# Kernel optimization log

Measured on AMD Instinct MI355X. Metric: run time of the kernel, lower is better.

Reference implementation:

```python
import jax, jax.numpy as jnp
import numpy as np
from jax import lax

H = 1024        # lstm_hidden_size
V = 512         # action_vocab_size
WV = 300        # word_vec_size
S = 64          # step_num
N = 512         # entity_num


def setup_inputs() -> dict:
    key = jax.random.key(0)
    ks = jax.random.split(key, 16)
    s = 0.02
    return {
        "video_vectors": jax.random.normal(ks[0], (1, S, H), jnp.float32),
        "entity_vectors": jax.random.normal(ks[1], (N, H), jnp.float32),
        # action_selector: Linear(H,H) -> ReLU -> Dropout(eval: identity) -> Linear(H,V) -> Sigmoid
        "A1w": jax.random.normal(ks[2], (H, H), jnp.float32) * s,
        "A1b": jnp.zeros((H,), jnp.float32),
        "A2w": jax.random.normal(ks[3], (V, H), jnp.float32) * s,
        "A2b": jnp.zeros((V,), jnp.float32),
        "action_emb": jax.random.normal(ks[4], (V, WV), jnp.float32) * s,
        "W1w": jax.random.normal(ks[5], (H, H), jnp.float32) * s,
        "W1b": jnp.zeros((H,), jnp.float32),
        "W2w": jax.random.normal(ks[6], (H, H + V), jnp.float32) * s,
        "W2b": jnp.zeros((H,), jnp.float32),
        "W3w": jax.random.normal(ks[7], (3, H), jnp.float32) * s,
        "W3b": jnp.zeros((3,), jnp.float32),
        "W4w": jax.random.normal(ks[8], (1, WV), jnp.float32) * s,
        "W4b": jnp.zeros((1,), jnp.float32),
    }


def _forward(video_vectors, entity_vectors, A1w, A1b, A2w, A2b, action_emb,
             W1w, W1b, W2w, W2b, W3w, W3b, W4w, W4b):
    vv = video_vectors[0]                       # [S, H]
    n = entity_vectors.shape[0]

    def step(carry, v_ac):
        ev, prev_ent_attn = carry               # ev: [N, H], prev: [N]
        # action selector (dropout is identity in eval)
        h = jax.nn.relu(v_ac @ A1w.T + A1b)
        ac_prob = jax.nn.sigmoid(h @ A2w.T + A2b)        # [V]
        bar_ft = (ac_prob / ac_prob.sum()) @ action_emb  # [WV]
        hat_ht = jax.nn.relu(v_ac @ W1w.T + W1b)         # [H]
        w2v = jnp.concatenate([hat_ht, ac_prob]) @ W2w.T + W2b  # [H]
        ent_prob = jax.nn.sigmoid(ev @ w2v)              # [N]
        choice = jax.nn.softmax(hat_ht @ W3w.T + W3b)    # [3]
        attn = choice[0] * ent_prob + choice[1] * prev_ent_attn  # (choice[2]*0)
        bar_et = (attn / attn.sum()) @ ev                # [H]
        scal = bar_ft @ W4w[0] + W4b[0]                  # scalar (W4(bar_ft))
        kt = jax.nn.relu(scal * bar_et)                  # [H]
        ev_new = attn[:, None] * kt[None, :] + (1.0 - attn)[:, None] * ev  # [N, H]
        return (ev_new, ent_prob), (ent_prob, ac_prob, bar_et, ev_new, bar_ft)

    init = (entity_vectors, jnp.zeros((n,), entity_vectors.dtype))
    _, (ent_probs, ac_probs, step_ent, step_all, step_act) = lax.scan(step, init, vv)
    return ent_probs, ac_probs, step_ent, step_all, step_act


def reference(video_vectors, entity_vectors, A1w, A1b, A2w, A2b, action_emb,
              W1w, W1b, W2w, W2b, W3w, W3b, W4w, W4b):
    return _forward(video_vectors, entity_vectors, A1w, A1b, A2w, A2b, action_emb,
                    W1w, W1b, W2w, W2b, W3w, W3b, W4w, W4b)
```

## Files before the change

### kernel.cpp

```cpp
#include <hip/hip_runtime.h>

#define H  1024
#define V  512
#define WV 300
#define S  64
#define N  512

#define WS_HALL   0
#define WS_CAT    (S*H)
#define WS_W2V    (WS_CAT + S*1536)
#define WS_CHOICE (WS_W2V + S*H)
#define WS_SCAL   (WS_CHOICE + 2*S)
#define WS_ACSUM  (WS_SCAL + S)
#define WS_KT     (WS_ACSUM + S)
#define WS_ATT    (WS_KT + S*H)
#define WS_ACCUM  (WS_ATT + S*N)
#define WS_ASUM   (WS_ACCUM + 3*H)
#define WS_CTR    (WS_ASUM + 4)

#define OUT_EP   0
#define OUT_AC   (S*N)
#define OUT_SE   (S*N + S*V)
#define OUT_ALL  (OUT_SE + S*H)
#define OUT_ACT  (OUT_ALL + (size_t)S*N*H)

__device__ __forceinline__ float wave_reduce(float v) {
#pragma unroll
  for (int m = 32; m > 0; m >>= 1) v += __shfl_xor(v, m, 64);
  return v;
}
__device__ __forceinline__ float dot4(float4 a, float4 b) {
  return a.x*b.x + a.y*b.y + a.z*b.z + a.w*b.w;
}

#define KC 64
__global__ __launch_bounds__(256) void gemmNT(
    const float* __restrict__ X, int ldx,
    const float* __restrict__ W, const float* __restrict__ bias,
    int K, int act,
    float* __restrict__ out1, int ld1,
    float* __restrict__ out2, int ld2) {
  __shared__ float Xs[64][KC + 4];
  __shared__ float Ws[64][KC + 4];
  const int tid = threadIdx.x;
  const int tm = tid >> 5, tn = tid & 31;
  const int jbase = blockIdx.x * 64;
  float acc[8][2];
#pragma unroll
  for (int i = 0; i < 8; ++i) acc[i][0] = acc[i][1] = 0.f;
  const int lr = tid >> 2;
  const int lc = (tid & 3) * 16;
  for (int k0 = 0; k0 < K; k0 += KC) {
    const float4* xp = (const float4*)(X + (size_t)lr * ldx + k0 + lc);
    const float4* wp = (const float4*)(W + (size_t)(jbase + lr) * K + k0 + lc);
    float4 xv0 = xp[0], xv1 = xp[1], xv2 = xp[2], xv3 = xp[3];
    float4 wv0 = wp[0], wv1 = wp[1], wv2 = wp[2], wv3 = wp[3];
    __syncthreads();
    *(float4*)&Xs[lr][lc +  0] = xv0; *(float4*)&Xs[lr][lc +  4] = xv1;
    *(float4*)&Xs[lr][lc +  8] = xv2; *(float4*)&Xs[lr][lc + 12] = xv3;
    *(float4*)&Ws[lr][lc +  0] = wv0; *(float4*)&Ws[lr][lc +  4] = wv1;
    *(float4*)&Ws[lr][lc +  8] = wv2; *(float4*)&Ws[lr][lc + 12] = wv3;
    __syncthreads();
#pragma unroll
    for (int kk = 0; kk < KC; kk += 4) {
      float4 w0 = *(const float4*)&Ws[tn][kk];
      float4 w1 = *(const float4*)&Ws[tn + 32][kk];
#pragma unroll
      for (int i = 0; i < 8; ++i) {
        float4 x = *(const float4*)&Xs[tm * 8 + i][kk];
        acc[i][0] += dot4(x, w0);
        acc[i][1] += dot4(x, w1);
      }
    }
  }
  const int j0 = jbase + tn, j1 = jbase + tn + 32;
  const float b0 = bias[j0], b1 = bias[j1];
#pragma unroll
  for (int i = 0; i < 8; ++i) {
    const int r = tm * 8 + i;
    float v0 = acc[i][0] + b0;
    float v1 = acc[i][1] + b1;
    if (act == 1) { v0 = fmaxf(v0, 0.f); v1 = fmaxf(v1, 0.f); }
    else if (act == 2) {
      v0 = 1.f / (1.f + __expf(-v0));
      v1 = 1.f / (1.f + __expf(-v1));
    }
    out1[(size_t)r * ld1 + j0] = v0;
    out1[(size_t)r * ld1 + j1] = v1;
    if (out2) {
      out2[(size_t)r * ld2 + j0] = v0;
      out2[(size_t)r * ld2 + j1] = v1;
    }
  }
}

__global__ void k_choice(const float* __restrict__ cat, const float* __restrict__ out_ac,
                         const float* __restrict__ W3w, const float* __restrict__ W3b,
                         float* __restrict__ ws) {
  int t = blockIdx.x, tid = threadIdx.x;
  const float* hat = cat + (size_t)t * 1536;
  float4 h4 = *(const float4*)(hat + tid * 4);
  float p[4];
#pragma unroll
  for (int r = 0; r < 3; ++r) {
    float4 w4 = *(const float4*)(W3w + (size_t)r * H + tid * 4);
    p[r] = dot4(h4, w4);
  }
  const float* ac = out_ac + (size_t)t * V;
  p[3] = ac[tid * 2] + ac[tid * 2 + 1];
  __shared__ float red[4][256];
#pragma unroll
  for (int q = 0; q < 4; ++q) red[q][tid] = p[q];
  __syncthreads();
  for (int sft = 128; sft > 0; sft >>= 1) {
    if (tid < sft) {
#pragma unroll
      for (int q = 0; q < 4; ++q) red[q][tid] += red[q][tid + sft];
    }
    __syncthreads();
  }
  if (tid == 0) {
    float l0 = red[0][0] + W3b[0], l1 = red[1][0] + W3b[1], l2 = red[2][0] + W3b[2];
    float m  = fmaxf(l0, fmaxf(l1, l2));
    float e0 = __expf(l0 - m), e1 = __expf(l1 - m), e2 = __expf(l2 - m);
    float inv = 1.f / (e0 + e1 + e2);
    ws[WS_CHOICE + t * 2]     = e0 * inv;
    ws[WS_CHOICE + t * 2 + 1] = e1 * inv;
    ws[WS_ACSUM + t]          = red[3][0];
  }
}

__global__ __launch_bounds__(256) void k_barft(
    const float* __restrict__ out_ac, const float* __restrict__ emb,
    const float* __restrict__ ws_ro, const float* __restrict__ W4w,
    const float* __restrict__ W4b, float* __restrict__ out_act,
    float* __restrict__ ws) {
  int t = blockIdx.x, tid = threadIdx.x;
  __shared__ float acS[V];
  const float* ac = out_ac + (size_t)t * V;
  acS[tid] = ac[tid];
  acS[tid + 256] = ac[tid + 256];
  __syncthreads();
  float s0 = 0.f, s1 = 0.f;
  const int w0 = tid, w1 = 256 + tid;
  for (int v = 0; v < V; ++v) {
    float a = acS[v];
    const float* er = emb + (size_t)v * WV;
    s0 += a * er[w0];
    if (tid < WV - 256) s1 += a * er[w1];
  }
  float inv = 1.f / ws_ro[WS_ACSUM + t];
  s0 *= inv; s1 *= inv;
  out_act[(size_t)t * WV + w0] = s0;
  if (tid < WV - 256) out_act[(size_t)t * WV + w1] = s1;
  float p = s0 * W4w[w0] + (tid < WV - 256 ? s1 * W4w[w1] : 0.f);
  __shared__ float red[256];
  red[tid] = p;
  __syncthreads();
  for (int s = 128; s > 0; s >>= 1) {
    if (tid < s) red[tid] += red[tid + s];
    __syncthreads();
  }
  if (tid == 0) ws[WS_SCAL + t] = red[0] + W4b[0];
}

__global__ __launch_bounds__(256) void k_seq(
    const float* __restrict__ ev0, const float* __restrict__ ws,
    float* __restrict__ accum, float* __restrict__ asum, unsigned* __restrict__ ctr,
    float* __restrict__ att, float* __restrict__ ktb,
    float* __restrict__ out_ep, float* __restrict__ out_se) {
  const int g = blockIdx.x, tid = threadIdx.x;
  const int lane = tid & 63, wv = tid >> 6;
  const int col = tid * 4;
  __shared__ float attnS[8], prevS[8], red[8][4];
  if (tid < 8) prevS[tid] = 0.f;
  float4 ev[8];
#pragma unroll
  for (int r = 0; r < 8; ++r)
    ev[r] = *(const float4*)(ev0 + (size_t)(g * 8 + r) * H + col);
  __syncthreads();
  unsigned target = 0;
  for (int t = 0; t < S; ++t) {
    const float4 w4 = *(const float4*)(ws + WS_W2V + (size_t)t * H + col);
    float dp[8];
#pragma unroll
    for (int r = 0; r < 8; ++r) dp[r] = dot4(ev[r], w4);
#pragma unroll
    for (int r = 0; r < 8; ++r) {
#pragma unroll
      for (int m = 32; m > 0; m >>= 1) dp[r] += __shfl_xor(dp[r], m, 64);
    }
    if (lane == 0) {
#pragma unroll
      for (int r = 0; r < 8; ++r) red[r][wv] = dp[r];
    }
    __syncthreads();
    if (tid < 8) {
      float d  = red[tid][0] + red[tid][1] + red[tid][2] + red[tid][3];
      float ep = 1.f / (1.f + __expf(-d));
      out_ep[(size_t)t * N + g * 8 + tid] = ep;
      float a = ws[WS_CHOICE + 2 * t] * ep + ws[WS_CHOICE + 2 * t + 1] * prevS[tid];
      prevS[tid] = ep;
      attnS[tid] = a;
      att[(size_t)t * N + g * 8 + tid] = a;
    }
    __syncthreads();
    float at[8];
#pragma unroll
    for (int r = 0; r < 8; ++r) at[r] = attnS[r];
    float4 pv = make_float4(0.f, 0.f, 0.f, 0.f);
#pragma unroll
    for (int r = 0; r < 8; ++r) {
      pv.x += at[r] * ev[r].x; pv.y += at[r] * ev[r].y;
      pv.z += at[r] * ev[r].z; pv.w += at[r] * ev[r].w;
    }
    float* acc = accum + (t % 3) * H;
    atomicAdd(acc + col + 0, pv.x);
    atomicAdd(acc + col + 1, pv.y);
    atomicAdd(acc + col + 2, pv.z);
    atomicAdd(acc + col + 3, pv.w);
    if (tid == 0) {
      float pa = 0.f;
#pragma unroll
      for (int r = 0; r < 8; ++r) pa += at[r];
      atomicAdd(asum + (t % 3), pa);
    }
    __syncthreads();
    target += (unsigned)gridDim.x;
    if (tid == 0) {
      __hip_atomic_fetch_add(ctr, 1u, __ATOMIC_RELEASE, __HIP_MEMORY_SCOPE_AGENT);
      while (__hip_atomic_load(ctr, __ATOMIC_ACQUIRE, __HIP_MEMORY_SCOPE_AGENT) < target)
        __builtin_amdgcn_s_sleep(2);
    }
    __syncthreads();
    float asv = __hip_atomic_load(asum + (t % 3), __ATOMIC_RELAXED, __HIP_MEMORY_SCOPE_AGENT);
    float4 pvs;
    pvs.x = __hip_atomic_load(acc + col + 0, __ATOMIC_RELAXED, __HIP_MEMORY_SCOPE_AGENT);
    pvs.y = __hip_atomic_load(acc + col + 1, __ATOMIC_RELAXED, __HIP_MEMORY_SCOPE_AGENT);
    pvs.z = __hip_atomic_load(acc + col + 2, __ATOMIC_RELAXED, __HIP_MEMORY_SCOPE_AGENT);
    pvs.w = __hip_atomic_load(acc + col + 3, __ATOMIC_RELAXED, __HIP_MEMORY_SCOPE_AGENT);
    float inv = 1.f / asv;
    float4 bar = make_float4(pvs.x * inv, pvs.y * inv, pvs.z * inv, pvs.w * inv);
    float sc = ws[WS_SCAL + t];
    float4 kt = make_float4(fmaxf(sc * bar.x, 0.f), fmaxf(sc * bar.y, 0.f),
                            fmaxf(sc * bar.z, 0.f), fmaxf(sc * bar.w, 0.f));
    if (g == 0) {
      *(float4*)(out_se + (size_t)t * H + col) = bar;
      *(float4*)(ktb + (size_t)t * H + col) = kt;
    }
    if (tid < 16)
      __hip_atomic_store(accum + ((t + 2) % 3) * H + g * 16 + tid, 0.f,
                         __ATOMIC_RELAXED, __HIP_MEMORY_SCOPE_AGENT);
    if (g == 0 && tid == 16)
      __hip_atomic_store(asum + ((t + 2) % 3), 0.f, __ATOMIC_RELAXED, __HIP_MEMORY_SCOPE_AGENT);
#pragma unroll
    for (int r = 0; r < 8; ++r) {
      float a = at[r];
      ev[r].x = a * kt.x + (1.f - a) * ev[r].x;
      ev[r].y = a * kt.y + (1.f - a) * ev[r].y;
      ev[r].z = a * kt.z + (1.f - a) * ev[r].z;
      ev[r].w = a * kt.w + (1.f - a) * ev[r].w;
    }
  }
}

__global__ __launch_bounds__(256) void k_recon(
    const float* __restrict__ ev0, const float* __restrict__ att,
    const float* __restrict__ ktb, float* __restrict__ out_all) {
  const int n = blockIdx.x, tid = threadIdx.x;
  const int col = tid * 4;
  __shared__ float aS[S];
  if (tid < S) aS[tid] = att[(size_t)tid * N + n];
  float4 v = *(const float4*)(ev0 + (size_t)n * H + col);
  __syncthreads();
  for (int t = 0; t < S; ++t) {
    float a = aS[t];
    float4 k4 = *(const float4*)(ktb + (size_t)t * H + col);
    v.x = a * k4.x + (1.f - a) * v.x;
    v.y = a * k4.y + (1.f - a) * v.y;
    v.z = a * k4.z + (1.f - a) * v.z;
    v.w = a * k4.w + (1.f - a) * v.w;
    *(float4*)(out_all + ((size_t)t * N + n) * H + col) = v;
  }
}

extern "C" void kernel_launch(void* const* d_in, const int* in_sizes, int n_in,
                              void* d_out, int out_size, void* d_ws, size_t ws_size,
                              hipStream_t stream) {
  const float* vv  = (const float*)d_in[0];
  const float* ev0 = (const float*)d_in[1];
  const float* A1w = (const float*)d_in[2];
  const float* A1b = (const float*)d_in[3];
  const float* A2w = (const float*)d_in[4];
  const float* A2b = (const float*)d_in[5];
  const float* emb = (const float*)d_in[6];
  const float* W1w = (const float*)d_in[7];
  const float* W1b = (const float*)d_in[8];
  const float* W2w = (const float*)d_in[9];
  const float* W2b = (const float*)d_in[10];
  const float* W3w = (const float*)d_in[11];
  const float* W3b = (const float*)d_in[12];
  const float* W4w = (const float*)d_in[13];
  const float* W4b = (const float*)d_in[14];

  float* ws  = (float*)d_ws;
  float* out = (float*)d_out;
  float* out_ep  = out + OUT_EP;
  float* out_ac  = out + OUT_AC;
  float* out_se  = out + OUT_SE;
  float* out_all = out + OUT_ALL;
  float* out_act = out + OUT_ACT;
  float* cat = ws + WS_CAT;

  hipMemsetAsync(ws + WS_ACCUM, 0, (size_t)(3 * H + 5) * sizeof(float), stream);

  gemmNT<<<16, 256, 0, stream>>>(vv, H, A1w, A1b, H, 1, ws + WS_HALL, H, (float*)nullptr, 0);
  gemmNT<<<16, 256, 0, stream>>>(vv, H, W1w, W1b, H, 1, cat, 1536, (float*)nullptr, 0);
  gemmNT<<<8, 256, 0, stream>>>(ws + WS_HALL, H, A2w, A2b, H, 2, out_ac, V, cat + H, 1536);
  k_choice<<<S, 256, 0, stream>>>(cat, out_ac, W3w, W3b, ws);
  gemmNT<<<16, 256, 0, stream>>>(cat, 1536, W2w, W2b, 1536, 0, ws + WS_W2V, H, (float*)nullptr, 0);
  k_barft<<<S, 256, 0, stream>>>(out_ac, emb, ws, W4w, W4b, out_act, ws);
  k_seq<<<64, 256, 0, stream>>>(ev0, ws, ws + WS_ACCUM, ws + WS_ASUM,
                                (unsigned*)(ws + WS_CTR),
                                ws + WS_ATT, ws + WS_KT, out_ep, out_se);
  k_recon<<<N, 256, 0, stream>>>(ev0, ws + WS_ATT, ws + WS_KT, out_all);
}
```

Before: 1.380 ms.

## Precompute entity-dot logits and update them algebraically in a column-split sequential kernel

Swaps the tiled GEMM kernels for wave-per-output dot-product kernels and adds a pass that precomputes ev0·w2v for every step. The sequential kernel now splits columns across blocks rather than entity rows. It keeps the future logits current through the recurrence D[n][t'] = a*(kt·w2v_t') + (1-a)*D[n][t'], so the per-step dot over the full entity matrix is no longer needed. Cross-block exchange uses per-block flags and published partials in place of float atomicAdd accumulation and a counter barrier. The cost is more spin-wait synchronisation points per step, plus extra grid-wide partial sums whose rounding order differs from the reference.

Result: slower. 1.579 ms (+14.4%).

```diff
diff --git a/kernel.cpp b/kernel.cpp
--- a/kernel.cpp
+++ b/kernel.cpp
@@ -14,9 +14,13 @@
 #define WS_ACSUM  (WS_SCAL + S)
 #define WS_KT     (WS_ACSUM + S)
 #define WS_ATT    (WS_KT + S*H)
-#define WS_ACCUM  (WS_ATT + S*N)
-#define WS_ASUM   (WS_ACCUM + 3*H)
-#define WS_CTR    (WS_ASUM + 4)
+#define WS_D0     (WS_ATT + S*N)
+#define WS_APUB   (WS_D0 + N*S)
+#define WS_GP1    (WS_APUB + 1024)
+#define WS_GBIG   (WS_GP1 + 128)
+#define WS_FLAGA  (WS_GBIG + 8192)
+#define WS_FLAGB  (WS_FLAGA + 64)
+#define WS_FLAGD  (WS_FLAGB + 64)
 
 #define OUT_EP   0
 #define OUT_AC   (S*N)
@@ -24,74 +28,89 @@
 #define OUT_ALL  (OUT_SE + S*H)
 #define OUT_ACT  (OUT_ALL + (size_t)S*N*H)
 
+#define RLX __ATOMIC_RELAXED
+#define AGT __HIP_MEMORY_SCOPE_AGENT
+
+__device__ __forceinline__ float dot4(float4 a, float4 b) {
+  return a.x*b.x + a.y*b.y + a.z*b.z + a.w*b.w;
+}
 __device__ __forceinline__ float wave_reduce(float v) {
 #pragma unroll
   for (int m = 32; m > 0; m >>= 1) v += __shfl_xor(v, m, 64);
   return v;
 }
-__device__ __forceinline__ float dot4(float4 a, float4 b) {
-  return a.x*b.x + a.y*b.y + a.z*b.z + a.w*b.w;
-}
-
-#define KC 64
-__global__ __launch_bounds__(256) void gemmNT(
-    const float* __restrict__ X, int ldx,
-    const float* __restrict__ W, const float* __restrict__ bias,
-    int K, int act,
-    float* __restrict__ out1, int ld1,
-    float* __restrict__ out2, int ld2) {
-  __shared__ float Xs[64][KC + 4];
-  __shared__ float Ws[64][KC + 4];
-  const int tid = threadIdx.x;
-  const int tm = tid >> 5, tn = tid & 31;
-  const int jbase = blockIdx.x * 64;
-  float acc[8][2];
-#pragma unroll
-  for (int i = 0; i < 8; ++i) acc[i][0] = acc[i][1] = 0.f;
-  const int lr = tid >> 2;
-  const int lc = (tid & 3) * 16;
-  for (int k0 = 0; k0 < K; k0 += KC) {
-    const float4* xp = (const float4*)(X + (size_t)lr * ldx + k0 + lc);
-    const float4* wp = (const float4*)(W + (size_t)(jbase + lr) * K + k0 + lc);
-    float4 xv0 = xp[0], xv1 = xp[1], xv2 = xp[2], xv3 = xp[3];
-    float4 wv0 = wp[0], wv1 = wp[1], wv2 = wp[2], wv3 = wp[3];
-    __syncthreads();
-    *(float4*)&Xs[lr][lc +  0] = xv0; *(float4*)&Xs[lr][lc +  4] = xv1;
-    *(float4*)&Xs[lr][lc +  8] = xv2; *(float4*)&Xs[lr][lc + 12] = xv3;
-    *(float4*)&Ws[lr][lc +  0] = wv0; *(float4*)&Ws[lr][lc +  4] = wv1;
-    *(float4*)&Ws[lr][lc +  8] = wv2; *(float4*)&Ws[lr][lc + 12] = wv3;
-    __syncthreads();
-#pragma unroll
-    for (int kk = 0; kk < KC; kk += 4) {
-      float4 w0 = *(const float4*)&Ws[tn][kk];
-      float4 w1 = *(const float4*)&Ws[tn + 32][kk];
-#pragma unroll
-      for (int i = 0; i < 8; ++i) {
-        float4 x = *(const float4*)&Xs[tm * 8 + i][kk];
-        acc[i][0] += dot4(x, w0);
-        acc[i][1] += dot4(x, w1);
-      }
-    }
-  }
-  const int j0 = jbase + tn, j1 = jbase + tn + 32;
-  const float b0 = bias[j0], b1 = bias[j1];
-#pragma unroll
-  for (int i = 0; i < 8; ++i) {
-    const int r = tm * 8 + i;
-    float v0 = acc[i][0] + b0;
-    float v1 = acc[i][1] + b1;
-    if (act == 1) { v0 = fmaxf(v0, 0.f); v1 = fmaxf(v1, 0.f); }
-    else if (act == 2) {
-      v0 = 1.f / (1.f + __expf(-v0));
-      v1 = 1.f / (1.f + __expf(-v1));
-    }
-    out1[(size_t)r * ld1 + j0] = v0;
-    out1[(size_t)r * ld1 + j1] = v1;
-    if (out2) {
-      out2[(size_t)r * ld2 + j0] = v0;
-      out2[(size_t)r * ld2 + j1] = v1;
-    }
-  }
+
+__global__ void k_vvmats(const float* __restrict__ vv,
+                         const float* __restrict__ A1w, const float* __restrict__ A1b,
+                         const float* __restrict__ W1w, const float* __restrict__ W1b,
+                         float* __restrict__ ws) {
+  int wid  = (blockIdx.x * 256 + threadIdx.x) >> 6;
+  int lane = threadIdx.x & 63;
+  int mat = wid >= H * S;
+  int rem = wid - mat * H * S;
+  int j = rem >> 6, t = rem & 63;
+  const float* w = (mat ? W1w : A1w) + (size_t)j * H;
+  const float* x = vv + (size_t)t * H;
+  float s = 0.f;
+#pragma unroll
+  for (int c = 0; c < 4; ++c)
+    s += dot4(*(const float4*)(w + c*256 + lane*4), *(const float4*)(x + c*256 + lane*4));
+  s = wave_reduce(s);
+  if (lane == 0) {
+    s = fmaxf(s + (mat ? W1b : A1b)[j], 0.f);
+    if (mat) ws[WS_CAT + (size_t)t * 1536 + j] = s;
+    else     ws[WS_HALL + (size_t)t * H + j] = s;
+  }
+}
+
+__global__ void k_ac(const float* __restrict__ ws_ro, const float* __restrict__ A2w,
+                     const float* __restrict__ A2b, float* __restrict__ out_ac,
+                     float* __restrict__ ws) {
+  int wid  = (blockIdx.x * 256 + threadIdx.x) >> 6;
+  int lane = threadIdx.x & 63;
+  int v = wid >> 6, t = wid & 63;
+  const float* x = ws_ro + WS_HALL + (size_t)t * H;
+  const float* w = A2w + (size_t)v * H;
+  float s = 0.f;
+#pragma unroll
+  for (int c = 0; c < 4; ++c)
+    s += dot4(*(const float4*)(w + c*256 + lane*4), *(const float4*)(x + c*256 + lane*4));
+  s = wave_reduce(s);
+  if (lane == 0) {
+    s = 1.f / (1.f + __expf(-(s + A2b[v])));
+    out_ac[(size_t)t * V + v] = s;
+    ws[WS_CAT + (size_t)t * 1536 + H + v] = s;
+  }
+}
+
+__global__ void k_w2v(const float* __restrict__ ws_ro, const float* __restrict__ W2w,
+                      const float* __restrict__ W2b, float* __restrict__ ws) {
+  int wid  = (blockIdx.x * 256 + threadIdx.x) >> 6;
+  int lane = threadIdx.x & 63;
+  int j = wid >> 6, t = wid & 63;
+  const float* x = ws_ro + WS_CAT + (size_t)t * 1536;
+  const float* w = W2w + (size_t)j * 1536;
+  float s = 0.f;
+#pragma unroll
+  for (int c = 0; c < 6; ++c)
+    s += dot4(*(const float4*)(w + c*256 + lane*4), *(const float4*)(x + c*256 + lane*4));
+  s = wave_reduce(s);
+  if (lane == 0) ws[WS_W2V + (size_t)t * H + j] = s + W2b[j];
+}
+
+__global__ void k_d0(const float* __restrict__ ev0, const float* __restrict__ ws_ro,
+                     float* __restrict__ D0out) {
+  int wid  = (blockIdx.x * 256 + threadIdx.x) >> 6;
+  int lane = threadIdx.x & 63;
+  int n = wid >> 6, t = wid & 63;
+  const float* x = ev0 + (size_t)n * H;
+  const float* w = ws_ro + WS_W2V + (size_t)t * H;
+  float s = 0.f;
+#pragma unroll
+  for (int c = 0; c < 4; ++c)
+    s += dot4(*(const float4*)(x + c*256 + lane*4), *(const float4*)(w + c*256 + lane*4));
+  s = wave_reduce(s);
+  if (lane == 0) D0out[wid] = s;
 }
 
 __global__ void k_choice(const float* __restrict__ cat, const float* __restrict__ out_ac,
@@ -102,10 +121,8 @@
   float4 h4 = *(const float4*)(hat + tid * 4);
   float p[4];
 #pragma unroll
-  for (int r = 0; r < 3; ++r) {
-    float4 w4 = *(const float4*)(W3w + (size_t)r * H + tid * 4);
-    p[r] = dot4(h4, w4);
-  }
+  for (int r = 0; r < 3; ++r)
+    p[r] = dot4(h4, *(const float4*)(W3w + (size_t)r * H + tid * 4));
   const float* ac = out_ac + (size_t)t * V;
   p[3] = ac[tid * 2] + ac[tid * 2 + 1];
   __shared__ float red[4][256];
@@ -166,101 +183,168 @@
 
 __global__ __launch_bounds__(256) void k_seq(
     const float* __restrict__ ev0, const float* __restrict__ ws,
-    float* __restrict__ accum, float* __restrict__ asum, unsigned* __restrict__ ctr,
+    const float* __restrict__ D0,
+    float* __restrict__ aPub, float* __restrict__ gp1, float* __restrict__ gbig,
+    int* __restrict__ flagA, int* __restrict__ flagB, int* __restrict__ flagD,
     float* __restrict__ att, float* __restrict__ ktb,
     float* __restrict__ out_ep, float* __restrict__ out_se) {
   const int g = blockIdx.x, tid = threadIdx.x;
-  const int lane = tid & 63, wv = tid >> 6;
-  const int col = tid * 4;
-  __shared__ float attnS[8], prevS[8], red[8][4];
-  if (tid < 8) prevS[tid] = 0.f;
-  float4 ev[8];
-#pragma unroll
-  for (int r = 0; r < 8; ++r)
-    ev[r] = *(const float4*)(ev0 + (size_t)(g * 8 + r) * H + col);
+  const int lane = tid & 63;
+  const int cg = tid & 15, ng = tid >> 4;
+  const int colbase = g * 16;
+  __shared__ float Dl[8][64];
+  __shared__ float aL[512];
+  __shared__ float red2[16][17];
+  __shared__ alignas(16) float ktL[16];
+  __shared__ float attnS[8], aOldS[8], prevS[8];
+  __shared__ float Grow[64];
+  __shared__ float asumS;
+  for (int i = tid; i < 512; i += 256)
+    Dl[i >> 6][i & 63] = D0[(size_t)(g * 8 + (i >> 6)) * 64 + (i & 63)];
+  if (tid < 8) { prevS[tid] = 0.f; attnS[tid] = 0.f; }
+  float evr[32];
+#pragma unroll
+  for (int i = 0; i < 32; ++i)
+    evr[i] = ev0[(size_t)(ng * 32 + i) * H + colbase + cg];
   __syncthreads();
-  unsigned target = 0;
+
   for (int t = 0; t < S; ++t) {
-    const float4 w4 = *(const float4*)(ws + WS_W2V + (size_t)t * H + col);
-    float dp[8];
-#pragma unroll
-    for (int r = 0; r < 8; ++r) dp[r] = dot4(ev[r], w4);
-#pragma unroll
-    for (int r = 0; r < 8; ++r) {
-#pragma unroll
-      for (int m = 32; m > 0; m >>= 1) dp[r] += __shfl_xor(dp[r], m, 64);
-    }
-    if (lane == 0) {
-#pragma unroll
-      for (int r = 0; r < 8; ++r) red[r][wv] = dp[r];
-    }
-    __syncthreads();
+    const int buf = t & 1;
     if (tid < 8) {
-      float d  = red[tid][0] + red[tid][1] + red[tid][2] + red[tid][3];
+      float d  = Dl[tid][t];
       float ep = 1.f / (1.f + __expf(-d));
       out_ep[(size_t)t * N + g * 8 + tid] = ep;
-      float a = ws[WS_CHOICE + 2 * t] * ep + ws[WS_CHOICE + 2 * t + 1] * prevS[tid];
+      float a = ws[WS_CHOICE + 2*t] * ep + ws[WS_CHOICE + 2*t + 1] * prevS[tid];
       prevS[tid] = ep;
+      aOldS[tid] = attnS[tid];
       attnS[tid] = a;
       att[(size_t)t * N + g * 8 + tid] = a;
-    }
-    __syncthreads();
-    float at[8];
-#pragma unroll
-    for (int r = 0; r < 8; ++r) at[r] = attnS[r];
-    float4 pv = make_float4(0.f, 0.f, 0.f, 0.f);
-#pragma unroll
-    for (int r = 0; r < 8; ++r) {
-      pv.x += at[r] * ev[r].x; pv.y += at[r] * ev[r].y;
-      pv.z += at[r] * ev[r].z; pv.w += at[r] * ev[r].w;
-    }
-    float* acc = accum + (t % 3) * H;
-    atomicAdd(acc + col + 0, pv.x);
-    atomicAdd(acc + col + 1, pv.y);
-    atomicAdd(acc + col + 2, pv.z);
-    atomicAdd(acc + col + 3, pv.w);
-    if (tid == 0) {
-      float pa = 0.f;
-#pragma unroll
-      for (int r = 0; r < 8; ++r) pa += at[r];
-      atomicAdd(asum + (t % 3), pa);
-    }
-    __syncthreads();
-    target += (unsigned)gridDim.x;
-    if (tid == 0) {
-      __hip_atomic_fetch_add(ctr, 1u, __ATOMIC_RELEASE, __HIP_MEMORY_SCOPE_AGENT);
-      while (__hip_atomic_load(ctr, __ATOMIC_ACQUIRE, __HIP_MEMORY_SCOPE_AGENT) < target)
-        __builtin_amdgcn_s_sleep(2);
-    }
-    __syncthreads();
-    float asv = __hip_atomic_load(asum + (t % 3), __ATOMIC_RELAXED, __HIP_MEMORY_SCOPE_AGENT);
-    float4 pvs;
-    pvs.x = __hip_atomic_load(acc + col + 0, __ATOMIC_RELAXED, __HIP_MEMORY_SCOPE_AGENT);
-    pvs.y = __hip_atomic_load(acc + col + 1, __ATOMIC_RELAXED, __HIP_MEMORY_SCOPE_AGENT);
-    pvs.z = __hip_atomic_load(acc + col + 2, __ATOMIC_RELAXED, __HIP_MEMORY_SCOPE_AGENT);
-    pvs.w = __hip_atomic_load(acc + col + 3, __ATOMIC_RELAXED, __HIP_MEMORY_SCOPE_AGENT);
-    float inv = 1.f / asv;
-    float4 bar = make_float4(pvs.x * inv, pvs.y * inv, pvs.z * inv, pvs.w * inv);
-    float sc = ws[WS_SCAL + t];
-    float4 kt = make_float4(fmaxf(sc * bar.x, 0.f), fmaxf(sc * bar.y, 0.f),
-                            fmaxf(sc * bar.z, 0.f), fmaxf(sc * bar.w, 0.f));
-    if (g == 0) {
-      *(float4*)(out_se + (size_t)t * H + col) = bar;
-      *(float4*)(ktb + (size_t)t * H + col) = kt;
-    }
-    if (tid < 16)
-      __hip_atomic_store(accum + ((t + 2) % 3) * H + g * 16 + tid, 0.f,
-                         __ATOMIC_RELAXED, __HIP_MEMORY_SCOPE_AGENT);
-    if (g == 0 && tid == 16)
-      __hip_atomic_store(asum + ((t + 2) % 3), 0.f, __ATOMIC_RELAXED, __HIP_MEMORY_SCOPE_AGENT);
-#pragma unroll
-    for (int r = 0; r < 8; ++r) {
-      float a = at[r];
-      ev[r].x = a * kt.x + (1.f - a) * ev[r].x;
-      ev[r].y = a * kt.y + (1.f - a) * ev[r].y;
-      ev[r].z = a * kt.z + (1.f - a) * ev[r].z;
-      ev[r].w = a * kt.w + (1.f - a) * ev[r].w;
-    }
+      __hip_atomic_store(aPub + buf * 512 + g * 8 + tid, a, RLX, AGT);
+    }
+    __threadfence();
+    __syncthreads();
+    if (tid == 0) __hip_atomic_store(flagA + g, t + 1, RLX, AGT);
+
+    if (t >= 1 && t < 63) {
+      const int pbuf = (t + 1) & 1;
+      if (tid < 64) {
+        for (;;) {
+          int f = __hip_atomic_load(flagD + lane, RLX, AGT);
+          if (__all(f >= t)) break;
+        }
+      }
+      __syncthreads();
+      int row = t + 1 + (tid >> 2);
+      float rs = 0.f;
+      if (row < 64) {
+        const float* p = gbig + ((size_t)pbuf * 64 + row) * 64 + (tid & 3) * 16;
+#pragma unroll
+        for (int i = 0; i < 16; ++i) rs += __hip_atomic_load(p + i, RLX, AGT);
+      }
+      rs += __shfl_xor(rs, 1, 64);
+      rs += __shfl_xor(rs, 2, 64);
+      if ((tid & 3) == 0 && row < 64) Grow[row] = rs;
+      __syncthreads();
+      {
+        int n = tid >> 5;
+        float ao = aOldS[n];
+        for (int r = (tid & 31) + t + 1; r < 64; r += 32)
+          Dl[n][r] = ao * Grow[r] + (1.f - ao) * Dl[n][r];
+      }
+      __syncthreads();
+    }
+
+    if (tid < 64) {
+      for (;;) {
+        int f = __hip_atomic_load(flagA + lane, RLX, AGT);
+        if (__all(f >= t + 1)) break;
+      }
+    }
+    __syncthreads();
+    aL[tid]       = __hip_atomic_load(aPub + buf * 512 + tid, RLX, AGT);
+    aL[tid + 256] = __hip_atomic_load(aPub + buf * 512 + 256 + tid, RLX, AGT);
+    __syncthreads();
+    if (tid < 64) {
+      float s = 0.f;
+      for (int i = lane; i < 512; i += 64) s += aL[i];
+      s = wave_reduce(s);
+      if (tid == 0) asumS = s;
+    }
+    float bp = 0.f;
+#pragma unroll
+    for (int i = 0; i < 32; ++i) bp += aL[ng * 32 + i] * evr[i];
+    red2[ng][cg] = bp;
+    __syncthreads();
+    if (tid < 16) {
+      float b = 0.f;
+#pragma unroll
+      for (int q = 0; q < 16; ++q) b += red2[q][tid];
+      b /= asumS;
+      float sc = ws[WS_SCAL + t];
+      float k  = fmaxf(sc * b, 0.f);
+      ktL[tid] = k;
+      out_se[(size_t)t * H + colbase + tid] = b;
+      ktb[(size_t)t * H + colbase + tid]    = k;
+    }
+    __syncthreads();
+    if (t < 63) {
+      if (tid < 16)
+        red2[0][tid] = ktL[tid] * ws[WS_W2V + (size_t)(t + 1) * H + colbase + tid];
+      __syncthreads();
+      if (tid == 0) {
+        float s = 0.f;
+#pragma unroll
+        for (int q = 0; q < 16; ++q) s += red2[0][q];
+        __hip_atomic_store(gp1 + buf * 64 + g, s, RLX, AGT);
+      }
+    }
+    {
+      float k = ktL[cg];
+#pragma unroll
+      for (int i = 0; i < 32; ++i) {
+        float a = aL[ng * 32 + i];
+        evr[i] = a * k + (1.f - a) * evr[i];
+      }
+    }
+    __threadfence();
+    __syncthreads();
+    if (tid == 0) __hip_atomic_store(flagB + g, t + 1, RLX, AGT);
+
+    if (t < 63) {
+      if (tid < 64) {
+        for (;;) {
+          int f = __hip_atomic_load(flagB + lane, RLX, AGT);
+          if (__all(f >= t + 1)) break;
+        }
+      }
+      __syncthreads();
+      if (tid < 64) {
+        float v = __hip_atomic_load(gp1 + buf * 64 + lane, RLX, AGT);
+        v = wave_reduce(v);
+        if (tid == 0) Grow[0] = v;
+      }
+      __syncthreads();
+      if (tid < 8) {
+        float a = attnS[tid];
+        Dl[tid][t + 1] = a * Grow[0] + (1.f - a) * Dl[tid][t + 1];
+      }
+    }
+
+    if (t < 62) {
+      int tp = t + 2 + (tid >> 2);
+      if (tp < 64) {
+        float4 w4 = *(const float4*)(ws + WS_W2V + (size_t)tp * H + colbase + (tid & 3) * 4);
+        float4 k4 = *(const float4*)&ktL[(tid & 3) * 4];
+        float s = dot4(w4, k4);
+        s += __shfl_xor(s, 1, 64);
+        s += __shfl_xor(s, 2, 64);
+        if ((tid & 3) == 0)
+          __hip_atomic_store(gbig + ((size_t)buf * 64 + tp) * 64 + g, s, RLX, AGT);
+      }
+    }
+    __threadfence();
+    __syncthreads();
+    if (tid == 0) __hip_atomic_store(flagD + g, t + 1, RLX, AGT);
   }
 }
 
@@ -312,16 +396,18 @@
   float* out_act = out + OUT_ACT;
   float* cat = ws + WS_CAT;
 
-  hipMemsetAsync(ws + WS_ACCUM, 0, (size_t)(3 * H + 5) * sizeof(float), stream);
-
-  gemmNT<<<16, 256, 0, stream>>>(vv, H, A1w, A1b, H, 1, ws + WS_HALL, H, (float*)nullptr, 0);
-  gemmNT<<<16, 256, 0, stream>>>(vv, H, W1w, W1b, H, 1, cat, 1536, (float*)nullptr, 0);
-  gemmNT<<<8, 256, 0, stream>>>(ws + WS_HALL, H, A2w, A2b, H, 2, out_ac, V, cat + H, 1536);
-  k_choice<<<S, 256, 0, stream>>>(cat, out_ac, W3w, W3b, ws);
-  gemmNT<<<16, 256, 0, stream>>>(cat, 1536, W2w, W2b, 1536, 0, ws + WS_W2V, H, (float*)nullptr, 0);
-  k_barft<<<S, 256, 0, stream>>>(out_ac, emb, ws, W4w, W4b, out_act, ws);
-  k_seq<<<64, 256, 0, stream>>>(ev0, ws, ws + WS_ACCUM, ws + WS_ASUM,
-                                (unsigned*)(ws + WS_CTR),
-                                ws + WS_ATT, ws + WS_KT, out_ep, out_se);
-  k_recon<<<N, 256, 0, stream>>>(ev0, ws + WS_ATT, ws + WS_KT, out_all);
-}
+  hipMemsetAsync(ws + WS_FLAGA, 0, 192 * sizeof(int), stream);
+
+  k_vvmats<<<(2 * H * S) / 4, 256, 0, stream>>>(vv, A1w, A1b, W1w, W1b, ws);
+  k_ac    <<<(V * S) / 4,     256, 0, stream>>>(ws, A2w, A2b, out_ac, ws);
+  k_choice<<<S,               256, 0, stream>>>(cat, out_ac, W3w, W3b, ws);
+  k_w2v   <<<(H * S) / 4,     256, 0, stream>>>(ws, W2w, W2b, ws);
+  k_d0    <<<(N * S) / 4,     256, 0, stream>>>(ev0, ws, ws + WS_D0);
+  k_barft <<<S,               256, 0, stream>>>(out_ac, emb, ws, W4w, W4b, out_act, ws);
+  k_seq   <<<64,              256, 0, stream>>>(ev0, ws, ws + WS_D0,
+                                                ws + WS_APUB, ws + WS_GP1, ws + WS_GBIG,
+                                                (int*)(ws + WS_FLAGA), (int*)(ws + WS_FLAGB),
+                                                (int*)(ws + WS_FLAGD),
+                                                ws + WS_ATT, ws + WS_KT, out_ep, out_se);
+  k_recon <<<N,               256, 0, stream>>>(ev0, ws + WS_ATT, ws + WS_KT, out_all);
+}
```
